# Kernel optimization log

Measured on AMD Instinct MI355X. Metric: run time of the kernel, lower is better.

## Reference

```python
import jax, jax.numpy as jnp
import numpy as np

V = 4
H, W, Z = 32, 64, 13
C = 256
NH = 8
WS = (4, 4, 1)
SS = (2, 2, 0)
HID = 1024


def _layernorm(x, g, b):
    mu = jnp.mean(x, axis=-1, keepdims=True)
    var = jnp.mean((x - mu) ** 2, axis=-1, keepdims=True)
    return (x - mu) * jax.lax.rsqrt(var + 1e-5) * g + b


def setup_inputs() -> dict:
    key = jax.random.key(0)
    ks = jax.random.split(key, 12)
    B = 2
    s = 0.02
    return {
        "x_z": jax.random.normal(ks[0], (B, H, W, Z, C), jnp.float32),
        "x_q": jax.random.normal(ks[1], (B, H, W, Z, C), jnp.float32),
        "x_t": jax.random.normal(ks[2], (B, H, W, Z, C), jnp.float32),
        "x_u": jax.random.normal(ks[3], (B, H, W, Z, C), jnp.float32),
        "qkv_w": jax.random.normal(ks[4], (V, C, 3 * C), jnp.float32) * s,
        "qkv_b": jnp.zeros((V, 3 * C), jnp.float32),
        "proj_w": jax.random.normal(ks[5], (V, C, C), jnp.float32) * s,
        "proj_b": jnp.zeros((V, C), jnp.float32),
        "n1_g": jnp.ones((V, C), jnp.float32),
        "n1_b": jnp.zeros((V, C), jnp.float32),
        "n2_g": jnp.ones((V, C), jnp.float32),
        "n2_b": jnp.zeros((V, C), jnp.float32),
        "fc1_w": jax.random.normal(ks[6], (V, C, HID), jnp.float32) * s,
        "fc1_b": jnp.zeros((V, HID), jnp.float32),
        "fc2_w": jax.random.normal(ks[7], (V, HID, C), jnp.float32) * s,
        "fc2_b": jnp.zeros((V, C), jnp.float32),
    }


def reference(x_z, x_q, x_t, x_u, qkv_w, qkv_b, proj_w, proj_b,
              n1_g, n1_b, n2_g, n2_b, fc1_w, fc1_b, fc2_w, fc2_b):
    x = jnp.stack([x_z, x_q, x_t, x_u], axis=0)  # [V,B,H,W,Z,C]
    B = x.shape[1]
    L = H * W * Z
    w0, w1, w2 = WS
    N = w0 * w1 * w2
    hd = C // NH
    scale = hd ** -0.5

    shortcut = x.reshape(V, B, L, C)
    xn = _layernorm(shortcut, n1_g[:, None, None, :], n1_b[:, None, None, :])
    xs = xn.reshape(V, B, H, W, Z, C)
    # cyclic shift (same sign used for both rolls in the source)
    xs = jnp.roll(xs, shift=SS, axis=(2, 3, 4))
    # window partition -> [V, B_, N, C]
    xw = xs.reshape(V, B, H // w0, w0, W // w1, w1, Z // w2, w2, C)
    xw = xw.transpose(0, 1, 2, 4, 6, 3, 5, 7, 8).reshape(V, -1, N, C)
    B_ = xw.shape[1]

    qkv = jnp.einsum('vbnc,vcd->vbnd', xw, qkv_w) + qkv_b[:, None, None, :]
    qkv = qkv.reshape(V, B_, N, 3, NH, hd).transpose(3, 1, 0, 4, 2, 5)  # [3,B_,V,NH,N,hd]
    q, k, v = qkv[0], qkv[1], qkv[2]
    # per-(variable, head) attention: heads of different variables are concatenated
    attn = jax.nn.softmax(jnp.einsum('bvhnd,bvhmd->bvhnm', q * scale, k), axis=-1)
    ctx = jnp.einsum('bvhnm,bvhmd->bvhnd', attn, v)  # [B_,V,NH,N,hd]
    # faithful to torch reshape (B_, N, V*NH, hd) -> (B_, V*N, C): rows interleave (n, v)
    big = ctx.transpose(0, 3, 1, 2, 4).reshape(B_, V * N, C)
    y = big.reshape(B_, V, N, C).transpose(1, 0, 2, 3)  # slice [:, i*N:(i+1)*N]
    y = jnp.einsum('vbnc,vcd->vbnd', y, proj_w) + proj_b[:, None, None, :]
    # window reverse
    y = y.reshape(V, B, H // w0, W // w1, Z // w2, w0, w1, w2, C)
    y = y.transpose(0, 1, 2, 5, 3, 6, 4, 7, 8).reshape(V, B, H, W, Z, C)
    y = jnp.roll(y, shift=SS, axis=(2, 3, 4))  # same-sign roll (preserves source behavior)
    y = y.reshape(V, B, L, C)

    x2 = shortcut + y
    xm = _layernorm(x2, n2_g[:, None, None, :], n2_b[:, None, None, :])
    h = jax.nn.gelu(jnp.einsum('vblc,vcd->vbld', xm, fc1_w) + fc1_b[:, None, None, :],
                    approximate=False)
    m = jnp.einsum('vbld,vdc->vblc', h, fc2_w) + fc2_b[:, None, None, :]
    out = (x2 + m).reshape(V, B, H, W, Z, C)
    return out  # stacked per-variable outputs in variable_order
```

## Files before the change

### kernel.cpp

```cpp
#include <hip/hip_runtime.h>
#include <hip/hip_bf16.h>
#include <cstdint>
#include <cstddef>

#define DI __device__ __forceinline__

typedef __bf16 bf16_t;
typedef bf16_t bf16x8 __attribute__((ext_vector_type(8)));
typedef float f32x4 __attribute__((ext_vector_type(4)));

constexpr int Vn = 4, Bn = 2, Hn = 32, Wn = 64, Zn = 13, Cn = 256, HIDn = 1024;
constexpr int Ln = Hn * Wn * Zn;
constexpr int BWn = Bn * (Hn / 4) * (Wn / 4) * Zn;
constexpr int PB = Bn * Ln;
constexpr int ROWS = Vn * PB;

DI void gload_lds16(const void* g, void* l) {
  __builtin_amdgcn_global_load_lds(
      (const __attribute__((address_space(1))) void*)g,
      (__attribute__((address_space(3))) void*)l, 16, 0, 0);
}

DI unsigned short f2bf_bits(float f) {
  __hip_bfloat16 h = __float2bfloat16(f);
  return *reinterpret_cast<unsigned short*>(&h);
}

DI float gelu_f(float x) {
  float u = x * x;
  float w = x * fmaf(0.044715f, u, 1.0f);
  float e = __expf(-1.5957691216057308f * w);
  return x * __builtin_amdgcn_rcpf(1.0f + e);
}

__global__ __launch_bounds__(256) void transpose_tile_kernel(
    const float* __restrict__ src, __hip_bfloat16* __restrict__ dst, int K, int N) {
  __shared__ float S[64][65];
  const int n0 = blockIdx.x * 64, k0 = blockIdx.y * 64, v = blockIdx.z;
  const int tc = threadIdx.x & 63, tr = threadIdx.x >> 6;
#pragma unroll
  for (int i = 0; i < 16; ++i) {
    int kk = tr + i * 4;
    S[kk][tc] = src[((size_t)v * K + k0 + kk) * N + n0 + tc];
  }
  __syncthreads();
#pragma unroll
  for (int i = 0; i < 16; ++i) {
    int nn = tr + i * 4;
    dst[((size_t)v * N + n0 + nn) * K + k0 + tc] = __float2bfloat16(S[tc][nn]);
  }
}

__global__ __launch_bounds__(256) void ln1_kernel(
    const float* __restrict__ x0, const float* __restrict__ x1,
    const float* __restrict__ x2i, const float* __restrict__ x3,
    const float* __restrict__ g_, const float* __restrict__ b_,
    __hip_bfloat16* __restrict__ xw) {
  int gw = blockIdx.x * 4 + (threadIdx.x >> 6);
  int lane = threadIdx.x & 63;
  int v = gw / PB;
  int rem = gw - v * PB;
  int bw = rem >> 4, nn = rem & 15;
  int zb = bw % 13;
  int t = bw / 13;
  int wb = t & 15, t2 = t >> 4;
  int hb = t2 & 7, b = t2 >> 3;
  int hs = (hb * 4 + (nn >> 2) + 30) & 31;
  int wsrc = (wb * 4 + (nn & 3) + 62) & 63;
  size_t l = (size_t)(hs * 64 + wsrc) * 13 + zb;
  const float* xv = (v == 0) ? x0 : (v == 1) ? x1 : (v == 2) ? x2i : x3;
  const float* xp = xv + ((size_t)b * Ln + l) * 256;
  float4 val = *(const float4*)(xp + lane * 4);
  float s = val.x + val.y + val.z + val.w;
  float sq = val.x * val.x + val.y * val.y + val.z * val.z + val.w * val.w;
#pragma unroll
  for (int o = 32; o; o >>= 1) {
    s += __shfl_xor(s, o);
    sq += __shfl_xor(sq, o);
  }
  float mean = s * (1.0f / 256.0f);
  float var = sq * (1.0f / 256.0f) - mean * mean;
  float rstd = rsqrtf(var + 1e-5f);
  const float* gg = g_ + v * 256 + lane * 4;
  const float* bb = b_ + v * 256 + lane * 4;
  ushort4 o4;
  o4.x = f2bf_bits((val.x - mean) * rstd * gg[0] + bb[0]);
  o4.y = f2bf_bits((val.y - mean) * rstd * gg[1] + bb[1]);
  o4.z = f2bf_bits((val.z - mean) * rstd * gg[2] + bb[2]);
  o4.w = f2bf_bits((val.w - mean) * rstd * gg[3] + bb[3]);
  *reinterpret_cast<ushort4*>(xw + (size_t)gw * 256 + lane * 4) = o4;
}

__global__ __launch_bounds__(256) void ln2_kernel(
    const float* __restrict__ x2, const float* __restrict__ g_,
    const float* __restrict__ b_, __hip_bfloat16* __restrict__ xm) {
  int r = blockIdx.x * 4 + (threadIdx.x >> 6);
  int lane = threadIdx.x & 63;
  int v = r / PB;
  const float* xp = x2 + (size_t)r * 256;
  float4 val = *(const float4*)(xp + lane * 4);
  float s = val.x + val.y + val.z + val.w;
  float sq = val.x * val.x + val.y * val.y + val.z * val.z + val.w * val.w;
#pragma unroll
  for (int o = 32; o; o >>= 1) {
    s += __shfl_xor(s, o);
    sq += __shfl_xor(sq, o);
  }
  float mean = s * (1.0f / 256.0f);
  float var = sq * (1.0f / 256.0f) - mean * mean;
  float rstd = rsqrtf(var + 1e-5f);
  const float* gg = g_ + v * 256 + lane * 4;
  const float* bb = b_ + v * 256 + lane * 4;
  ushort4 o4;
  o4.x = f2bf_bits((val.x - mean) * rstd * gg[0] + bb[0]);
  o4.y = f2bf_bits((val.y - mean) * rstd * gg[1] + bb[1]);
  o4.z = f2bf_bits((val.z - mean) * rstd * gg[2] + bb[2]);
  o4.w = f2bf_bits((val.w - mean) * rstd * gg[3] + bb[3]);
  *reinterpret_cast<ushort4*>(xm + (size_t)r * 256 + lane * 4) = o4;
}

__global__ __launch_bounds__(256) void attn_kernel(
    const __hip_bfloat16* __restrict__ qkvp, __hip_bfloat16* __restrict__ ctx) {
  __shared__ float P[4][16][17];
  int b_ = blockIdx.x;
  int v = blockIdx.y;
  int wid = threadIdx.x >> 6, lane = threadIdx.x & 63;
  int lm = lane & 15, hi = lane >> 4;
  const bf16_t* base = (const bf16_t*)qkvp + (size_t)(v * BWn + b_) * 16 * 768;
  const float scale = 0.17677669529663687f;
  f32x4 zero = {0.f, 0.f, 0.f, 0.f};
#pragma unroll
  for (int hh = 0; hh < 2; ++hh) {
    int h = wid + 4 * hh;
    bf16x8 qf = *(const bf16x8*)(base + (size_t)lm * 768 + h * 32 + hi * 8);
    bf16x8 kf = *(const bf16x8*)(base + (size_t)lm * 768 + 256 + h * 32 + hi * 8);
    f32x4 s = __builtin_amdgcn_mfma_f32_16x16x32_bf16(qf, kf, zero, 0, 0, 0);
    float p0[4];
#pragma unroll
    for (int q = 0; q < 4; ++q) {
      float val = s[q] * scale;
      float mx = val;
#pragma unroll
      for (int o = 8; o >= 1; o >>= 1) mx = fmaxf(mx, __shfl_xor(mx, o));
      float e = __expf(val - mx);
      float sum = e;
#pragma unroll
      for (int o = 8; o >= 1; o >>= 1) sum += __shfl_xor(sum, o);
      p0[q] = e * __builtin_amdgcn_rcpf(sum);
    }
#pragma unroll
    for (int q = 0; q < 4; ++q) P[wid][hi * 4 + q][lm] = p0[q];
    bf16x8 pa;
#pragma unroll
    for (int j = 0; j < 8; ++j) pa[j] = (bf16_t)0.f;
    if (hi < 2) {
#pragma unroll
      for (int j = 0; j < 8; ++j) pa[j] = (bf16_t)P[wid][lm][hi * 8 + j];
    }
#pragma unroll
    for (int dh = 0; dh < 2; ++dh) {
      bf16x8 vf;
#pragma unroll
      for (int j = 0; j < 8; ++j) vf[j] = (bf16_t)0.f;
      if (hi < 2) {
#pragma unroll
        for (int j = 0; j < 8; ++j)
          vf[j] = base[(size_t)(hi * 8 + j) * 768 + 512 + h * 32 + dh * 16 + lm];
      }
      f32x4 c = __builtin_amdgcn_mfma_f32_16x16x32_bf16(pa, vf, zero, 0, 0, 0);
#pragma unroll
      for (int q = 0; q < 4; ++q) {
        int n = hi * 4 + q;
        int d = dh * 16 + lm;
        int r = n * 4 + v;
        int vo = r >> 4, no = r & 15;
        ctx[((size_t)(vo * BWn + b_) * 16 + no) * 256 + h * 32 + d] = __float2bfloat16(c[q]);
      }
    }
  }
}

template <int EPI, int K, int N>
__global__ __launch_bounds__(512, 4) void gemm5(
    const __hip_bfloat16* __restrict__ A, const __hip_bfloat16* __restrict__ WT,
    const float* __restrict__ bias, __hip_bfloat16* __restrict__ outb,
    float* __restrict__ outf, const float* __restrict__ xi0,
    const float* __restrict__ xi1, const float* __restrict__ xi2,
    const float* __restrict__ xi3) {
  constexpr int NT = K / 64;
  constexpr int NC = N / 256;
  const int v = blockIdx.z;
  const int x = blockIdx.x;
  const int xcd = x & 7;
  const int j = x >> 3;
  const int c = j % NC;
  const int r = xcd + 8 * (j / NC);
  const int rowBase = r * 128;
  const int colBase = c * 256;

  const bf16_t* Av = (const bf16_t*)A + ((size_t)v * PB + rowBase) * K;
  const bf16_t* Wv = (const bf16_t*)WT + ((size_t)v * N + colBase) * K;

  __shared__ __align__(16) uint8_t smem[49152];
  bf16_t(*As)[64] = (bf16_t(*)[64])smem;
  bf16_t(*Bs)[64] = (bf16_t(*)[64])(smem + 16384);

  const int tid = threadIdx.x, wid = tid >> 6, lane = tid & 63;
  const int wr = wid >> 2, wc = wid & 3;
  const int lm = lane & 15, hi = lane >> 4;
  const int rA = lane >> 3;
  const int lg = (lane & 7) ^ rA;

  f32x4 acc[4][4];
#pragma unroll
  for (int m = 0; m < 4; ++m)
#pragma unroll
    for (int n = 0; n < 4; ++n) acc[m][n] = f32x4{0.f, 0.f, 0.f, 0.f};

  for (int t = 0; t < NT; ++t) {
    if (t) __syncthreads();
#pragma unroll
    for (int g = 0; g < 2; ++g) {
      int grp = wid * 2 + g;
      gload_lds16(Av + (size_t)(grp * 8 + rA) * K + t * 64 + lg * 8, &As[grp * 8][0]);
    }
#pragma unroll
    for (int g = 0; g < 4; ++g) {
      int grp = wid * 4 + g;
      gload_lds16(Wv + (size_t)(grp * 8 + rA) * K + t * 64 + lg * 8, &Bs[grp * 8][0]);
    }
    __syncthreads();
#pragma unroll
    for (int kk = 0; kk < 2; ++kk) {
      bf16x8 af[4], bfv[4];
#pragma unroll
      for (int m = 0; m < 4; ++m) {
        const int rr = wr * 64 + m * 16 + lm;
        af[m] = *(const bf16x8*)&As[rr][((kk * 4 + hi) ^ (lm & 7)) * 8];
      }
#pragma unroll
      for (int n = 0; n < 4; ++n) {
        const int rr = wc * 64 + n * 16 + lm;
        bfv[n] = *(const bf16x8*)&Bs[rr][((kk * 4 + hi) ^ (lm & 7)) * 8];
      }
#pragma unroll
      for (int m = 0; m < 4; ++m)
#pragma unroll
        for (int n = 0; n < 4; ++n)
          acc[m][n] = __builtin_amdgcn_mfma_f32_16x16x32_bf16(af[m], bfv[n], acc[m][n], 0, 0, 0);
    }
  }

  __syncthreads();
  uint8_t* ep = smem + wid * 6144;
  const int pr = lane >> 3, pc = lane & 7;

  if constexpr (EPI == 0 || EPI == 2) {
    ushort(*E)[72] = (ushort(*)[72])ep;
    float bcol[4];
#pragma unroll
    for (int n = 0; n < 4; ++n) bcol[n] = bias[v * N + colBase + wc * 64 + n * 16 + lm];
#pragma unroll
    for (int ph = 0; ph < 2; ++ph) {
#pragma unroll
      for (int mm = 0; mm < 2; ++mm) {
        int m = ph * 2 + mm;
#pragma unroll
        for (int q = 0; q < 4; ++q) {
          int lr = mm * 16 + hi * 4 + q;
#pragma unroll
          for (int n = 0; n < 4; ++n) {
            float val = acc[m][n][q] + bcol[n];
            if constexpr (EPI == 2) val = gelu_f(val);
            E[lr][n * 16 + lm] = f2bf_bits(val);
          }
        }
      }
#pragma unroll
      for (int p = 0; p < 4; ++p) {
        int lr = p * 8 + pr;
        bf16x8 valv = *(const bf16x8*)&E[lr][pc * 8];
        size_t grow = (size_t)v * PB + rowBase + wr * 64 + ph * 32 + lr;
        int gcol = colBase + wc * 64 + pc * 8;
        *(bf16x8*)&outb[grow * N + gcol] = valv;
      }
    }
  } else {
    float(*F)[36] = (float(*)[36])ep;
#pragma unroll
    for (int ph = 0; ph < 2; ++ph) {
#pragma unroll
      for (int h2 = 0; h2 < 2; ++h2) {
#pragma unroll
        for (int mm = 0; mm < 2; ++mm) {
          int m = ph * 2 + mm;
#pragma unroll
          for (int q = 0; q < 4; ++q) {
            int lr = mm * 16 + hi * 4 + q;
#pragma unroll
            for (int n2 = 0; n2 < 2; ++n2) F[lr][n2 * 16 + lm] = acc[m][h2 * 2 + n2][q];
          }
        }
#pragma unroll
        for (int p = 0; p < 4; ++p) {
          int lr = p * 8 + pr;
          f32x4 a4 = *(const f32x4*)&F[lr][pc * 4];
          int rowv = rowBase + wr * 64 + ph * 32 + lr;
          int gcol = colBase + wc * 64 + h2 * 32 + pc * 4;
          f32x4 b4 = *(const f32x4*)&bias[v * N + gcol];
          if constexpr (EPI == 1) {
            int b_ = rowv >> 4, nn = rowv & 15;
            int zb = b_ % 13;
            int tt = b_ / 13;
            int wb = tt & 15, tt2 = tt >> 4;
            int hb = tt2 & 7, bb = tt2 >> 3;
            int h2v = (hb * 4 + (nn >> 2) + 2) & 31;
            int w2v = (wb * 4 + (nn & 3) + 2) & 63;
            size_t l = (size_t)(h2v * 64 + w2v) * 13 + zb;
            const float* xv = (v == 0) ? xi0 : (v == 1) ? xi1 : (v == 2) ? xi2 : xi3;
            f32x4 x4 = *(const f32x4*)(xv + ((size_t)bb * Ln + l) * 256 + gcol);
            f32x4 o4 = a4 + b4 + x4;
            *(f32x4*)(outf + (((size_t)v * Bn + bb) * Ln + l) * 256 + gcol) = o4;
          } else {
            float* o = outf + ((size_t)v * PB + rowv) * 256 + gcol;
            f32x4 cur = *(const f32x4*)o;
            f32x4 o4 = cur + a4 + b4;
            *(f32x4*)o = o4;
          }
        }
      }
    }
  }
}

extern "C" void kernel_launch(void* const* d_in, const int* in_sizes, int n_in,
                              void* d_out, int out_size, void* d_ws, size_t ws_size,
                              hipStream_t stream) {
  const float* x0 = (const float*)d_in[0];
  const float* x1 = (const float*)d_in[1];
  const float* x2i = (const float*)d_in[2];
  const float* x3 = (const float*)d_in[3];
  const float* qkv_w = (const float*)d_in[4];
  const float* qkv_b = (const float*)d_in[5];
  const float* proj_w = (const float*)d_in[6];
  const float* proj_b = (const float*)d_in[7];
  const float* n1g = (const float*)d_in[8];
  const float* n1b = (const float*)d_in[9];
  const float* n2g = (const float*)d_in[10];
  const float* n2b = (const float*)d_in[11];
  const float* fc1_w = (const float*)d_in[12];
  const float* fc1_b = (const float*)d_in[13];
  const float* fc2_w = (const float*)d_in[14];
  const float* fc2_b = (const float*)d_in[15];
  float* out = (float*)d_out;

  uint8_t* ws = (uint8_t*)d_ws;
  size_t off = 0;
  auto alloc = [&](size_t bytes) -> void* {
    void* p = ws + off;
    off += (bytes + 255) & ~(size_t)255;
    return p;
  };
  __hip_bfloat16* wqkvT = (__hip_bfloat16*)alloc((size_t)Vn * Cn * 768 * 2);
  __hip_bfloat16* wprojT = (__hip_bfloat16*)alloc((size_t)Vn * Cn * Cn * 2);
  __hip_bfloat16* wfc1T = (__hip_bfloat16*)alloc((size_t)Vn * Cn * HIDn * 2);
  __hip_bfloat16* wfc2T = (__hip_bfloat16*)alloc((size_t)Vn * HIDn * Cn * 2);
  __hip_bfloat16* xw = (__hip_bfloat16*)alloc((size_t)ROWS * Cn * 2);
  __hip_bfloat16* qkvb = (__hip_bfloat16*)alloc((size_t)ROWS * HIDn * 2);

  transpose_tile_kernel<<<dim3(768 / 64, 256 / 64, Vn), 256, 0, stream>>>(qkv_w, wqkvT, 256, 768);
  transpose_tile_kernel<<<dim3(256 / 64, 256 / 64, Vn), 256, 0, stream>>>(proj_w, wprojT, 256, 256);
  transpose_tile_kernel<<<dim3(1024 / 64, 256 / 64, Vn), 256, 0, stream>>>(fc1_w, wfc1T, 256, 1024);
  transpose_tile_kernel<<<dim3(256 / 64, 1024 / 64, Vn), 256, 0, stream>>>(fc2_w, wfc2T, 1024, 256);

  ln1_kernel<<<ROWS / 4, 256, 0, stream>>>(x0, x1, x2i, x3, n1g, n1b, xw);

  gemm5<0, 256, 768><<<dim3(416 * 3, 1, Vn), 512, 0, stream>>>(
      xw, wqkvT, qkv_b, qkvb, nullptr, nullptr, nullptr, nullptr, nullptr);

  attn_kernel<<<dim3(BWn, Vn), 256, 0, stream>>>(qkvb, xw );

  gemm5<1, 256, 256><<<dim3(416, 1, Vn), 512, 0, stream>>>(
      xw , wprojT, proj_b, nullptr, out , x0, x1, x2i, x3);

  ln2_kernel<<<ROWS / 4, 256, 0, stream>>>(out , n2g, n2b, xw );

  gemm5<2, 256, 1024><<<dim3(416 * 4, 1, Vn), 512, 0, stream>>>(
      xw , wfc1T, fc1_b, qkvb , nullptr, nullptr, nullptr, nullptr, nullptr);

  gemm5<3, 1024, 256><<<dim3(416, 1, Vn), 512, 0, stream>>>(
      qkvb , wfc2T, fc2_b, nullptr, out, nullptr, nullptr, nullptr, nullptr);
}
```

Before: 1.007 ms.

## Double-buffer GEMM LDS tiles and enlarge row tile to 256

The GEMM kernel now uses a 256x256 output tile per block (each wave computes 128x64) with a K-step of 32, and double-buffers the A/B tiles in LDS so the next slice's global-to-LDS loads are issued before the current slice's MFMAs. This aims to hide global load latency behind compute and to raise operand reuse per loaded tile. In exchange it doubles accumulator registers, drops the occupancy hint from 4 to 2 blocks, uses 64KB of LDS, and halves the grid size, which may reduce latency hiding from other blocks and leave fewer blocks to spread across CUs.

```diff
diff --git a/kernel.cpp b/kernel.cpp
--- a/kernel.cpp
+++ b/kernel.cpp
@@ -181,78 +181,78 @@
 }
 
 template <int EPI, int K, int N>
-__global__ __launch_bounds__(512, 4) void gemm5(
+__global__ __launch_bounds__(512, 2) void gemm6(
     const __hip_bfloat16* __restrict__ A, const __hip_bfloat16* __restrict__ WT,
     const float* __restrict__ bias, __hip_bfloat16* __restrict__ outb,
     float* __restrict__ outf, const float* __restrict__ xi0,
     const float* __restrict__ xi1, const float* __restrict__ xi2,
     const float* __restrict__ xi3) {
-  constexpr int NT = K / 64;
+  constexpr int NT = K / 32;
   constexpr int NC = N / 256;
   const int v = blockIdx.z;
   const int x = blockIdx.x;
   const int xcd = x & 7;
   const int j = x >> 3;
   const int c = j % NC;
-  const int r = xcd + 8 * (j / NC);
-  const int rowBase = r * 128;
+  const int rp = xcd + 8 * (j / NC);
+  const int rowBase = rp * 256;
   const int colBase = c * 256;
 
   const bf16_t* Av = (const bf16_t*)A + ((size_t)v * PB + rowBase) * K;
   const bf16_t* Wv = (const bf16_t*)WT + ((size_t)v * N + colBase) * K;
 
-  __shared__ __align__(16) uint8_t smem[49152];
-  bf16_t(*As)[64] = (bf16_t(*)[64])smem;
-  bf16_t(*Bs)[64] = (bf16_t(*)[64])(smem + 16384);
+  __shared__ __align__(16) uint8_t smem[65536];
 
   const int tid = threadIdx.x, wid = tid >> 6, lane = tid & 63;
   const int wr = wid >> 2, wc = wid & 3;
   const int lm = lane & 15, hi = lane >> 4;
-  const int rA = lane >> 3;
-  const int lg = (lane & 7) ^ rA;
-
-  f32x4 acc[4][4];
-#pragma unroll
-  for (int m = 0; m < 4; ++m)
+  const int rS = lane >> 2;
+  const int gS = (lane & 3) ^ (rS & 3);
+
+  f32x4 acc[8][4];
+#pragma unroll
+  for (int m = 0; m < 8; ++m)
 #pragma unroll
     for (int n = 0; n < 4; ++n) acc[m][n] = f32x4{0.f, 0.f, 0.f, 0.f};
 
+  auto stage = [&](int buf, int t) {
+    bf16_t* Ad = (bf16_t*)(smem + buf * 16384);
+    bf16_t* Bd = (bf16_t*)(smem + 32768 + buf * 16384);
+#pragma unroll
+    for (int g = 0; g < 2; ++g) {
+      int r0 = (wid * 2 + g) * 16;
+      gload_lds16(Av + (size_t)(r0 + rS) * K + t * 32 + gS * 8, Ad + r0 * 32);
+    }
+#pragma unroll
+    for (int g = 0; g < 2; ++g) {
+      int r0 = (wid * 2 + g) * 16;
+      gload_lds16(Wv + (size_t)(r0 + rS) * K + t * 32 + gS * 8, Bd + r0 * 32);
+    }
+  };
+
+  stage(0, 0);
+  __syncthreads();
+
   for (int t = 0; t < NT; ++t) {
-    if (t) __syncthreads();
-#pragma unroll
-    for (int g = 0; g < 2; ++g) {
-      int grp = wid * 2 + g;
-      gload_lds16(Av + (size_t)(grp * 8 + rA) * K + t * 64 + lg * 8, &As[grp * 8][0]);
-    }
-#pragma unroll
-    for (int g = 0; g < 4; ++g) {
-      int grp = wid * 4 + g;
-      gload_lds16(Wv + (size_t)(grp * 8 + rA) * K + t * 64 + lg * 8, &Bs[grp * 8][0]);
+    const int cur = t & 1;
+    if (t + 1 < NT) stage(cur ^ 1, t + 1);
+    const bf16_t* Ab = (const bf16_t*)(smem + cur * 16384);
+    const bf16_t* Bb = (const bf16_t*)(smem + 32768 + cur * 16384);
+    bf16x8 bfv[4];
+#pragma unroll
+    for (int n = 0; n < 4; ++n)
+      bfv[n] = *(const bf16x8*)&Bb[(wc * 64 + n * 16 + lm) * 32 + (hi ^ (lm & 3)) * 8];
+#pragma unroll
+    for (int m = 0; m < 8; ++m) {
+      bf16x8 af = *(const bf16x8*)&Ab[(wr * 128 + m * 16 + lm) * 32 + (hi ^ (lm & 3)) * 8];
+#pragma unroll
+      for (int n = 0; n < 4; ++n)
+        acc[m][n] = __builtin_amdgcn_mfma_f32_16x16x32_bf16(af, bfv[n], acc[m][n], 0, 0, 0);
     }
     __syncthreads();
-#pragma unroll
-    for (int kk = 0; kk < 2; ++kk) {
-      bf16x8 af[4], bfv[4];
-#pragma unroll
-      for (int m = 0; m < 4; ++m) {
-        const int rr = wr * 64 + m * 16 + lm;
-        af[m] = *(const bf16x8*)&As[rr][((kk * 4 + hi) ^ (lm & 7)) * 8];
-      }
-#pragma unroll
-      for (int n = 0; n < 4; ++n) {
-        const int rr = wc * 64 + n * 16 + lm;
-        bfv[n] = *(const bf16x8*)&Bs[rr][((kk * 4 + hi) ^ (lm & 7)) * 8];
-      }
-#pragma unroll
-      for (int m = 0; m < 4; ++m)
-#pragma unroll
-        for (int n = 0; n < 4; ++n)
-          acc[m][n] = __builtin_amdgcn_mfma_f32_16x16x32_bf16(af[m], bfv[n], acc[m][n], 0, 0, 0);
-    }
-  }
-
-  __syncthreads();
-  uint8_t* ep = smem + wid * 6144;
+  }
+
+  uint8_t* ep = smem + wid * 8192;
   const int pr = lane >> 3, pc = lane & 7;
 
   if constexpr (EPI == 0 || EPI == 2) {
@@ -261,7 +261,7 @@
 #pragma unroll
     for (int n = 0; n < 4; ++n) bcol[n] = bias[v * N + colBase + wc * 64 + n * 16 + lm];
 #pragma unroll
-    for (int ph = 0; ph < 2; ++ph) {
+    for (int ph = 0; ph < 4; ++ph) {
 #pragma unroll
       for (int mm = 0; mm < 2; ++mm) {
         int m = ph * 2 + mm;
@@ -280,7 +280,7 @@
       for (int p = 0; p < 4; ++p) {
         int lr = p * 8 + pr;
         bf16x8 valv = *(const bf16x8*)&E[lr][pc * 8];
-        size_t grow = (size_t)v * PB + rowBase + wr * 64 + ph * 32 + lr;
+        size_t grow = (size_t)v * PB + rowBase + wr * 128 + ph * 32 + lr;
         int gcol = colBase + wc * 64 + pc * 8;
         *(bf16x8*)&outb[grow * N + gcol] = valv;
       }
@@ -288,7 +288,7 @@
   } else {
     float(*F)[36] = (float(*)[36])ep;
 #pragma unroll
-    for (int ph = 0; ph < 2; ++ph) {
+    for (int ph = 0; ph < 4; ++ph) {
 #pragma unroll
       for (int h2 = 0; h2 < 2; ++h2) {
 #pragma unroll
@@ -305,7 +305,7 @@
         for (int p = 0; p < 4; ++p) {
           int lr = p * 8 + pr;
           f32x4 a4 = *(const f32x4*)&F[lr][pc * 4];
-          int rowv = rowBase + wr * 64 + ph * 32 + lr;
+          int rowv = rowBase + wr * 128 + ph * 32 + lr;
           int gcol = colBase + wc * 64 + h2 * 32 + pc * 4;
           f32x4 b4 = *(const f32x4*)&bias[v * N + gcol];
           if constexpr (EPI == 1) {
@@ -323,8 +323,8 @@
             *(f32x4*)(outf + (((size_t)v * Bn + bb) * Ln + l) * 256 + gcol) = o4;
           } else {
             float* o = outf + ((size_t)v * PB + rowv) * 256 + gcol;
-            f32x4 cur = *(const f32x4*)o;
-            f32x4 o4 = cur + a4 + b4;
+            f32x4 cur4 = *(const f32x4*)o;
+            f32x4 o4 = cur4 + a4 + b4;
             *(f32x4*)o = o4;
           }
         }
@@ -375,19 +375,19 @@
 
   ln1_kernel<<<ROWS / 4, 256, 0, stream>>>(x0, x1, x2i, x3, n1g, n1b, xw);
 
-  gemm5<0, 256, 768><<<dim3(416 * 3, 1, Vn), 512, 0, stream>>>(
+  gemm6<0, 256, 768><<<dim3(208 * 3, 1, Vn), 512, 0, stream>>>(
       xw, wqkvT, qkv_b, qkvb, nullptr, nullptr, nullptr, nullptr, nullptr);
 
   attn_kernel<<<dim3(BWn, Vn), 256, 0, stream>>>(qkvb, xw );
 
-  gemm5<1, 256, 256><<<dim3(416, 1, Vn), 512, 0, stream>>>(
+  gemm6<1, 256, 256><<<dim3(208, 1, Vn), 512, 0, stream>>>(
       xw , wprojT, proj_b, nullptr, out , x0, x1, x2i, x3);
 
   ln2_kernel<<<ROWS / 4, 256, 0, stream>>>(out , n2g, n2b, xw );
 
-  gemm5<2, 256, 1024><<<dim3(416 * 4, 1, Vn), 512, 0, stream>>>(
+  gemm6<2, 256, 1024><<<dim3(208 * 4, 1, Vn), 512, 0, stream>>>(
       xw , wfc1T, fc1_b, qkvb , nullptr, nullptr, nullptr, nullptr, nullptr);
 
-  gemm5<3, 1024, 256><<<dim3(416, 1, Vn), 512, 0, stream>>>(
+  gemm6<3, 1024, 256><<<dim3(208, 1, Vn), 512, 0, stream>>>(
       qkvb , wfc2T, fc2_b, nullptr, out, nullptr, nullptr, nullptr, nullptr);
 }
```

Result: slower. 1.033 ms (+2.6%).
